# Optimization experiments

Measured on AMD Instinct MI355X. Metric: run time of the kernel, lower is better.

The kernel has to match this reference:

```python
import jax, jax.numpy as jnp
import numpy as np


def _hat(w):
    wx, wy, wz = w[..., 0], w[..., 1], w[..., 2]
    O = jnp.zeros_like(wx)
    return jnp.stack([
        jnp.stack([O, -wz, wy], -1),
        jnp.stack([wz, O, -wx], -1),
        jnp.stack([-wy, wx, O], -1)], -2)


def so3_exp_map(w):
    # w: [B,3] axis-angle -> [B,3,3] rotation (Rodrigues with Taylor fallback)
    th2 = jnp.sum(w * w, -1)[..., None, None]
    th = jnp.sqrt(th2 + 1e-30)
    a = jnp.where(th2 > 1e-8, jnp.sin(th) / th, 1.0 - th2 / 6.0)
    b = jnp.where(th2 > 1e-8, (1.0 - jnp.cos(th)) / th2, 0.5 - th2 / 24.0)
    K = _hat(w)
    I = jnp.eye(3, dtype=w.dtype)
    return I + a * K + b * (K @ K)


def _trilinear(vol, pts):
    # vol: [X,Y,Z]; pts: [N,3] voxel coords; zero outside the volume
    dims = jnp.asarray(vol.shape, dtype=pts.dtype)
    inside = jnp.all((pts >= 0.0) & (pts <= dims - 1.0), axis=-1)
    p0 = jnp.floor(pts)
    f = pts - p0
    hi = jnp.asarray(vol.shape, dtype=jnp.int32) - 1
    i0 = jnp.clip(p0.astype(jnp.int32), 0, hi)
    i1 = jnp.clip(i0 + 1, 0, hi)
    x0, y0, z0 = i0[:, 0], i0[:, 1], i0[:, 2]
    x1, y1, z1 = i1[:, 0], i1[:, 1], i1[:, 2]
    fx, fy, fz = f[:, 0], f[:, 1], f[:, 2]
    gx, gy, gz = 1.0 - fx, 1.0 - fy, 1.0 - fz
    val = (vol[x0, y0, z0] * gx * gy * gz + vol[x1, y0, z0] * fx * gy * gz
           + vol[x0, y1, z0] * gx * fy * gz + vol[x0, y0, z1] * gx * gy * fz
           + vol[x1, y1, z0] * fx * fy * gz + vol[x1, y0, z1] * fx * gy * fz
           + vol[x0, y1, z1] * gx * fy * fz + vol[x1, y1, z1] * fx * fy * fz)
    return jnp.where(inside, val, 0.0)


def setup_inputs() -> dict:
    key = jax.random.key(0)
    k1, k2, k3 = jax.random.split(key, 3)
    D = 256
    volume = jax.random.uniform(k1, (D, D, D), dtype=jnp.float32)
    spacing = jnp.ones(3, dtype=jnp.float32)                    # 1 mm voxels
    origin = jnp.full((3,), -(D - 1) / 2.0, dtype=jnp.float32)  # volume centered at 0
    isocenter = jnp.zeros(3, dtype=jnp.float32)
    sdd = jnp.array([1020.0], dtype=jnp.float32)
    # cam-to-world: source 510 mm behind isocenter on -z axis
    rt_inv = jnp.eye(4, dtype=jnp.float32).at[2, 3].set(-510.0)[None]
    # intrinsics: 512x512 detector, 2 mm pixels -> focal = sdd/pixel = 510
    f = 510.0
    K = jnp.array([[f, 0.0, 256.0], [0.0, f, 256.0], [0.0, 0.0, 1.0]], jnp.float32)
    k_inv = jnp.linalg.inv(K)
    eps = 1e-8
    rot = eps * jax.random.normal(k2, (1, 3), dtype=jnp.float32)
    xyz = eps * jax.random.normal(k3, (1, 3), dtype=jnp.float32)
    return {"volume": volume, "rt_inv": rt_inv, "k_inv": k_inv, "sdd": sdd,
            "isocenter": isocenter, "origin": origin, "spacing": spacing,
            "rot": rot, "xyz": xyz, "height": 512, "width": 512, "n_steps": 256}


def reference(volume, rt_inv, k_inv, sdd, isocenter, origin, spacing, rot, xyz,
              height, width, n_steps):
    dtype = volume.dtype
    # --- pose property: pivot @ exp(rot),R@xyz @ pivot_inv, then rt_inv @ pose ---
    R = so3_exp_map(rot)[0]                       # [3,3]
    t = R @ xyz[0]                                # einsum('bij,bj->bi')
    T = jnp.eye(4, dtype=dtype).at[:3, :3].set(R).at[:3, 3].set(t)
    rtm = rt_inv[0]
    c = (jnp.linalg.inv(rtm) @ jnp.append(isocenter, jnp.ones(1, dtype)))[:3]
    piv = jnp.eye(4, dtype=dtype).at[:3, 3].set(c)
    piv_inv = jnp.eye(4, dtype=dtype).at[:3, 3].set(-c)
    pose = rtm @ (piv @ (T @ piv_inv))            # cam-to-world, [4,4]
    # --- render: ray-march DRR ---
    u = jnp.arange(width, dtype=dtype) + 0.5
    v = jnp.arange(height, dtype=dtype) + 0.5
    uu, vv = jnp.meshgrid(u, v, indexing='xy')    # [H,W]
    pix = jnp.stack([uu.ravel(), vv.ravel(), jnp.ones(height * width, dtype)], -1)
    dir_cam = (pix @ k_inv.T) * sdd[0]            # detector points at depth sdd, cam frame
    Rw, src = pose[:3, :3], pose[:3, 3]
    dirs = dir_cam @ Rw.T                         # world-frame source->detector rays [N,3]
    seglen = jnp.linalg.norm(dirs, axis=-1) / n_steps

    def step(acc, i):
        frac = (i.astype(dtype) + 0.5) / n_steps
        pts = src + dirs * frac                   # [N,3] world points
        vox = (pts - origin) / spacing            # voxel coords
        return acc + _trilinear(volume, vox), None

    acc, _ = jax.lax.scan(step, jnp.zeros(height * width, dtype), jnp.arange(n_steps))
    img = acc * seglen                            # line-integral approximation
    return img.reshape(1, 1, height, width)
```

## Files before the change

kernel.cpp:

```cpp
#include <hip/hip_runtime.h>
#include <hip/hip_fp16.h>

#define W 512
#define H 512
#define NSTEPS 256
#define D 256
#define DM1 255.0f
#define PAIR_WS_BYTES (256ull*256ull*256ull*4ull)

struct SetupOut {
    float Rw[9];
    float src[3];
    float kinv[9];
    float sdd;
    float org[3];
    float invsp[3];
};

__device__ __forceinline__ void mat4mul(const float* A, const float* B, float* C) {
    #pragma unroll
    for (int i = 0; i < 4; ++i)
        #pragma unroll
        for (int j = 0; j < 4; ++j) {
            float s = 0.f;
            #pragma unroll
            for (int k = 0; k < 4; ++k) s += A[i*4+k] * B[k*4+j];
            C[i*4+j] = s;
        }
}

__device__ void compute_setup(const float* rt_inv, const float* k_inv, const float* sdd,
                              const float* isocenter, const float* origin, const float* spacing,
                              const float* rot, const float* xyz, SetupOut* o) {
    float wx = rot[0], wy = rot[1], wz = rot[2];
    float th2 = wx*wx + wy*wy + wz*wz;
    float th = sqrtf(th2 + 1e-30f);
    float a, b;
    if (th2 > 1e-8f) { a = sinf(th) / th; b = (1.f - cosf(th)) / th2; }
    else             { a = 1.f - th2 / 6.f; b = 0.5f - th2 / 24.f; }
    float K[9]  = {0.f,-wz,wy,  wz,0.f,-wx,  -wy,wx,0.f};
    float K2[9];
    #pragma unroll
    for (int i = 0; i < 3; ++i)
        #pragma unroll
        for (int j = 0; j < 3; ++j) {
            float s = 0.f;
            #pragma unroll
            for (int k = 0; k < 3; ++k) s += K[i*3+k] * K[k*3+j];
            K2[i*3+j] = s;
        }
    float R[9];
    #pragma unroll
    for (int i = 0; i < 9; ++i) R[i] = ((i % 4 == 0) ? 1.f : 0.f) + a*K[i] + b*K2[i];
    float t[3];
    #pragma unroll
    for (int i = 0; i < 3; ++i)
        t[i] = R[i*3+0]*xyz[0] + R[i*3+1]*xyz[1] + R[i*3+2]*xyz[2];

    float Ainv[16];
    const float* M = rt_inv;
    if (M[12] == 0.f && M[13] == 0.f && M[14] == 0.f && M[15] == 1.f) {
        const float r00=M[0],r01=M[1],r02=M[2],  r10=M[4],r11=M[5],r12=M[6],
                    r20=M[8],r21=M[9],r22=M[10];
        const float c00 = r11*r22 - r12*r21, c01 = r02*r21 - r01*r22, c02 = r01*r12 - r02*r11;
        const float c10 = r12*r20 - r10*r22, c11 = r00*r22 - r02*r20, c12 = r02*r10 - r00*r12;
        const float c20 = r10*r21 - r11*r20, c21 = r01*r20 - r00*r21, c22 = r00*r11 - r01*r10;
        const float det = r00*c00 + r01*c10 + r02*c20;
        const float id  = 1.f / det;
        const float tx = M[3], ty = M[7], tz = M[11];
        Ainv[0]=c00*id; Ainv[1]=c01*id; Ainv[2]=c02*id;
        Ainv[4]=c10*id; Ainv[5]=c11*id; Ainv[6]=c12*id;
        Ainv[8]=c20*id; Ainv[9]=c21*id; Ainv[10]=c22*id;
        Ainv[3]  = -(Ainv[0]*tx + Ainv[1]*ty + Ainv[2]*tz);
        Ainv[7]  = -(Ainv[4]*tx + Ainv[5]*ty + Ainv[6]*tz);
        Ainv[11] = -(Ainv[8]*tx + Ainv[9]*ty + Ainv[10]*tz);
        Ainv[12]=0.f; Ainv[13]=0.f; Ainv[14]=0.f; Ainv[15]=1.f;
    } else {
        float A[16];
        #pragma unroll
        for (int i = 0; i < 16; ++i) { A[i] = rt_inv[i]; Ainv[i] = 0.f; }
        Ainv[0] = Ainv[5] = Ainv[10] = Ainv[15] = 1.f;
        for (int c = 0; c < 4; ++c) {
            int p = c; float mx = fabsf(A[c*4+c]);
            for (int r = c+1; r < 4; ++r) { float v = fabsf(A[r*4+c]); if (v > mx) { mx = v; p = r; } }
            if (p != c) {
                for (int j = 0; j < 4; ++j) {
                    float tmp = A[c*4+j];   A[c*4+j]   = A[p*4+j];   A[p*4+j]   = tmp;
                    tmp = Ainv[c*4+j];      Ainv[c*4+j] = Ainv[p*4+j]; Ainv[p*4+j] = tmp;
                }
            }
            float inv = 1.f / A[c*4+c];
            for (int j = 0; j < 4; ++j) { A[c*4+j] *= inv; Ainv[c*4+j] *= inv; }
            for (int r = 0; r < 4; ++r) if (r != c) {
                float f = A[r*4+c];
                for (int j = 0; j < 4; ++j) { A[r*4+j] -= f*A[c*4+j]; Ainv[r*4+j] -= f*Ainv[c*4+j]; }
            }
        }
    }
    float cv[3];
    #pragma unroll
    for (int i = 0; i < 3; ++i)
        cv[i] = Ainv[i*4+0]*isocenter[0] + Ainv[i*4+1]*isocenter[1]
              + Ainv[i*4+2]*isocenter[2] + Ainv[i*4+3];

    float T[16]    = {R[0],R[1],R[2],t[0],  R[3],R[4],R[5],t[1],  R[6],R[7],R[8],t[2],  0,0,0,1};
    float piv[16]  = {1,0,0, cv[0],  0,1,0, cv[1],  0,0,1, cv[2],  0,0,0,1};
    float pivi[16] = {1,0,0,-cv[0],  0,1,0,-cv[1],  0,0,1,-cv[2],  0,0,0,1};
    float M1[16], M2[16], pose[16];
    mat4mul(T, pivi, M1);
    mat4mul(piv, M1, M2);
    mat4mul(rt_inv, M2, pose);

    #pragma unroll
    for (int i = 0; i < 3; ++i) {
        #pragma unroll
        for (int j = 0; j < 3; ++j) o->Rw[i*3+j] = pose[i*4+j];
        o->src[i] = pose[i*4+3];
    }
    #pragma unroll
    for (int i = 0; i < 9; ++i) o->kinv[i] = k_inv[i];
    o->sdd = sdd[0];
    #pragma unroll
    for (int i = 0; i < 3; ++i) { o->org[i] = origin[i]; o->invsp[i] = 1.f / spacing[i]; }
}

__global__ __launch_bounds__(256) void setup_kernel2(
    const float* __restrict__ rt_inv, const float* __restrict__ k_inv,
    const float* __restrict__ sdd, const float* __restrict__ isocenter,
    const float* __restrict__ origin, const float* __restrict__ spacing,
    const float* __restrict__ rot, const float* __restrict__ xyz,
    SetupOut* __restrict__ sp, unsigned char* __restrict__ gmask)
{
    __shared__ SetupOut S;
    if (threadIdx.x == 0) {
        compute_setup(rt_inv, k_inv, sdd, isocenter, origin, spacing, rot, xyz, &S);
        *sp = S;
    }
    __syncthreads();
    if (!gmask) return;

    __shared__ unsigned char m[256];
    m[threadIdx.x] = 0;
    __syncthreads();
    {
        const int i = threadIdx.x;
        const float frac = ((float)i + 0.5f) * (1.0f / (float)NSTEPS);
        const float Az = (S.src[2] - S.org[2]) * S.invsp[2];
        float vmin = 1e30f, vmax = -1e30f;
        #pragma unroll
        for (int c = 0; c < 4; ++c) {
            const float u = (c & 1)  ? ((float)W - 0.5f) : 0.5f;
            const float v = (c >> 1) ? ((float)H - 0.5f) : 0.5f;
            const float dcx = (S.kinv[0]*u + S.kinv[1]*v + S.kinv[2]) * S.sdd;
            const float dcy = (S.kinv[3]*u + S.kinv[4]*v + S.kinv[5]) * S.sdd;
            const float dcz = (S.kinv[6]*u + S.kinv[7]*v + S.kinv[8]) * S.sdd;
            const float dz  = S.Rw[6]*dcx + S.Rw[7]*dcy + S.Rw[8]*dcz;
            const float Bz  = dz * S.invsp[2];
            const float vz  = fmaf(Bz, frac, Az);
            vmin = fminf(vmin, vz);
            vmax = fmaxf(vmax, vz);
        }
        const int zlo = max(0,     (int)floorf(vmin - 0.05f));
        const int zhi = min(D - 1, (int)floorf(vmax + 0.05f) + 1);
        for (int z = zlo; z <= zhi; ++z) m[z] = 1;
    }
    __syncthreads();
    gmask[threadIdx.x] = m[threadIdx.x];
}

__global__ __launch_bounds__(256) void repack_pair_t(const float* __restrict__ vol,
                                                     unsigned int* __restrict__ ws,
                                                     const unsigned char* __restrict__ gmask) {
    const int x  = blockIdx.x;
    const int y0 = blockIdx.y * 128;
    const int z0 = blockIdx.z * 64;
    const int tid  = threadIdx.x;

    __shared__ unsigned int tf2[129 * 32];
    __shared__ unsigned char zm[64];
    const int xbase = x << 16;

    if (tid < 64) zm[tid] = gmask ? gmask[z0 + tid] : (unsigned char)1;

    {
        const int s  = tid & 31;
        const int r0 = tid >> 5;
        const bool need = (gmask == nullptr) ||
                          (gmask[z0 + 2*s] | gmask[z0 + 2*s + 1]) != 0;
        if (need) {
            for (int r = r0; r <= 128; r += 8) {
                const int y = min(y0 + r, D - 1);
                const float2 f = reinterpret_cast<const float2*>(vol + xbase + (y << 8) + z0)[s];
                __half2 h = __floats2half2_rn(f.x, f.y);
                tf2[r * 32 + (s ^ (r & 31))] = *reinterpret_cast<unsigned int*>(&h);
            }
        }
    }
    __syncthreads();

    const int grp  = tid >> 6;
    const int lane = tid & 63;
    const int ra = 2 * lane, rb = 2 * lane + 1, rc = 2 * lane + 2;
    for (int w = grp; w < 64; w += 4) {
        if (!zm[w]) continue;
        const int wp = w >> 1;
        const int sh = (w & 1) << 4;
        const unsigned int ha = (tf2[ra * 32 + (wp ^ (ra & 31))] >> sh) & 0xffffu;
        const unsigned int hb = (tf2[rb * 32 + (wp ^ (rb & 31))] >> sh) & 0xffffu;
        const unsigned int hc = (tf2[rc * 32 + (wp ^ (rc & 31))] >> sh) & 0xffffu;
        uint2 q;
        q.x = ha | (hb << 16);
        q.y = hb | (hc << 16);
        *reinterpret_cast<uint2*>(ws + xbase + ((z0 + w) << 8) + y0 + ra) = q;
    }
}

struct RayState {
    float Ax, Ay, Az, Bx, By, Bz, seglen;
    int imin, imax;
    bool any;
};

__device__ __forceinline__ RayState ray_setup(const SetupOut* S, int ix, int iy) {
    RayState r;
    const float u = (float)ix + 0.5f;
    const float v = (float)iy + 0.5f;
    const float dcx = (S->kinv[0]*u + S->kinv[1]*v + S->kinv[2]) * S->sdd;
    const float dcy = (S->kinv[3]*u + S->kinv[4]*v + S->kinv[5]) * S->sdd;
    const float dcz = (S->kinv[6]*u + S->kinv[7]*v + S->kinv[8]) * S->sdd;
    const float dx = S->Rw[0]*dcx + S->Rw[1]*dcy + S->Rw[2]*dcz;
    const float dy = S->Rw[3]*dcx + S->Rw[4]*dcy + S->Rw[5]*dcz;
    const float dz = S->Rw[6]*dcx + S->Rw[7]*dcy + S->Rw[8]*dcz;
    r.seglen = sqrtf(dx*dx + dy*dy + dz*dz) * (1.0f / (float)NSTEPS);
    r.Ax = (S->src[0] - S->org[0]) * S->invsp[0];
    r.Ay = (S->src[1] - S->org[1]) * S->invsp[1];
    r.Az = (S->src[2] - S->org[2]) * S->invsp[2];
    r.Bx = dx * S->invsp[0];
    r.By = dy * S->invsp[1];
    r.Bz = dz * S->invsp[2];

    float fmin = 0.f, fmax = 1.f;
    bool empty = false;
    const float aa[3] = { r.Ax, r.Ay, r.Az };
    const float bb[3] = { r.Bx, r.By, r.Bz };
    #pragma unroll
    for (int k = 0; k < 3; ++k) {
        if (fabsf(bb[k]) > 1e-12f) {
            const float rcp = 1.f / bb[k];
            const float t0 = (0.f - aa[k]) * rcp;
            const float t1 = (DM1 - aa[k]) * rcp;
            fmin = fmaxf(fmin, fminf(t0, t1));
            fmax = fminf(fmax, fmaxf(t0, t1));
        } else if (aa[k] < 0.f || aa[k] > DM1) {
            empty = true;
        }
    }
    r.any = !empty && (fmax >= fmin);
    r.imin = max(0,          (int)floorf(fmin * (float)NSTEPS - 0.5f) - 1);
    r.imax = min(NSTEPS - 1, (int)ceilf (fmax * (float)NSTEPS - 0.5f) + 1);
    return r;
}

__global__ __launch_bounds__(256) void drr_pair_kernel(
    const unsigned int* __restrict__ wsp, const SetupOut* __restrict__ S,
    float* __restrict__ out)
{
    const int b   = blockIdx.x;
    const int xcd = b & 7;
    const int j   = b >> 3;
    const int uu  = xcd * 16 + (j & 15);
    const int vv  = j >> 4;

    const int seg = threadIdx.x & 3;
    const int iy = vv * 16 + (threadIdx.x >> 2);
    const int ix = uu * 4  + threadIdx.y;
    const RayState r = ray_setup(S, ix, iy);

    float acc = 0.f;
    if (r.any) {
        #pragma unroll 4
        for (int i = r.imin + seg; i <= r.imax; i += 4) {
            const float frac = ((float)i + 0.5f) * (1.0f / (float)NSTEPS);
            const float vx = fmaf(r.Bx, frac, r.Ax);
            const float vy = fmaf(r.By, frac, r.Ay);
            const float vz = fmaf(r.Bz, frac, r.Az);
            const bool inside = (vx >= 0.f) && (vx <= DM1) &&
                                (vy >= 0.f) && (vy <= DM1) &&
                                (vz >= 0.f) && (vz <= DM1);
            const float cx = fminf(fmaxf(vx, 0.f), DM1);
            const float cy = fminf(fmaxf(vy, 0.f), DM1);
            const float cz = fminf(fmaxf(vz, 0.f), DM1);
            const float px = floorf(cx), py = floorf(cy), pz = floorf(cz);
            const int x0 = (int)px, y0 = (int)py, z0 = (int)pz;
            const int x1 = min(x0 + 1, D - 1);
            const int z1 = min(z0 + 1, D - 1);
            const float fx = cx - px, fy = cy - py, fz = cz - pz;
            const float gx = 1.f - fx, gy = 1.f - fy, gz = 1.f - fz;

            const int e00 = (x0 << 16) + (z0 << 8) + y0;
            const int zo  = (z1 - z0) << 8;
            const int xo  = (x1 - x0) << 16;

            const unsigned int q00 = wsp[e00];
            const unsigned int q01 = wsp[e00 + zo];
            const unsigned int q10 = wsp[e00 + xo];
            const unsigned int q11 = wsp[e00 + xo + zo];

            const float2 a00 = __half22float2(*reinterpret_cast<const __half2*>(&q00));
            const float2 a01 = __half22float2(*reinterpret_cast<const __half2*>(&q01));
            const float2 a10 = __half22float2(*reinterpret_cast<const __half2*>(&q10));
            const float2 a11 = __half22float2(*reinterpret_cast<const __half2*>(&q11));

            const float m00 = a00.x*gy + a00.y*fy;
            const float m01 = a01.x*gy + a01.y*fy;
            const float m10 = a10.x*gy + a10.y*fy;
            const float m11 = a11.x*gy + a11.y*fy;
            const float c0 = m00*gz + m01*fz;
            const float c1 = m10*gz + m11*fz;
            const float samp = c0*gx + c1*fx;
            acc += inside ? samp : 0.f;
        }
    }
    acc += __shfl_xor(acc, 1);
    acc += __shfl_xor(acc, 2);
    if (seg == 0)
        out[iy * W + ix] = acc * r.seglen;
}

__global__ __launch_bounds__(256) void drr_direct_kernel(
    const float* __restrict__ vol,
    const float* __restrict__ rt_inv, const float* __restrict__ k_inv,
    const float* __restrict__ sdd, const float* __restrict__ isocenter,
    const float* __restrict__ origin, const float* __restrict__ spacing,
    const float* __restrict__ rot, const float* __restrict__ xyz,
    float* __restrict__ out)
{
    __shared__ SetupOut S;
    if (threadIdx.x == 0 && threadIdx.y == 0)
        compute_setup(rt_inv, k_inv, sdd, isocenter, origin, spacing, rot, xyz, &S);
    __syncthreads();

    const int seg = threadIdx.x & 1;
    const int iy = blockIdx.x * 32 + (threadIdx.x >> 1);
    const int ix = blockIdx.y * 4  + threadIdx.y;
    const RayState r = ray_setup(&S, ix, iy);

    float acc = 0.f;
    if (r.any) {
        #pragma unroll 4
        for (int i = r.imin + seg; i <= r.imax; i += 2) {
            const float frac = ((float)i + 0.5f) * (1.0f / (float)NSTEPS);
            const float vx = fmaf(r.Bx, frac, r.Ax);
            const float vy = fmaf(r.By, frac, r.Ay);
            const float vz = fmaf(r.Bz, frac, r.Az);
            const bool inside = (vx >= 0.f) && (vx <= DM1) &&
                                (vy >= 0.f) && (vy <= DM1) &&
                                (vz >= 0.f) && (vz <= DM1);
            const float cx = fminf(fmaxf(vx, 0.f), DM1);
            const float cy = fminf(fmaxf(vy, 0.f), DM1);
            const float cz = fminf(fmaxf(vz, 0.f), DM1);
            const float px = floorf(cx), py = floorf(cy), pz = floorf(cz);
            const int x0 = (int)px, y0 = (int)py, z0 = (int)pz;
            const int x1 = min(x0 + 1, D - 1);
            const int y1 = min(y0 + 1, D - 1);
            const int z1 = min(z0 + 1, D - 1);
            const float fx = cx - px, fy = cy - py, fz = cz - pz;
            const float gx = 1.f - fx, gy = 1.f - fy, gz = 1.f - fz;

            const int base = (x0 << 16) + (y0 << 8);
            const int bx = (x1 - x0) << 16;
            const int by = (y1 - y0) << 8;

            const float v000 = vol[base + z0],           v001 = vol[base + z1];
            const float v010 = vol[base + by + z0],      v011 = vol[base + by + z1];
            const float v100 = vol[base + bx + z0],      v101 = vol[base + bx + z1];
            const float v110 = vol[base + bx + by + z0], v111 = vol[base + bx + by + z1];

            const float c00 = v000*gz + v001*fz;
            const float c01 = v010*gz + v011*fz;
            const float c10 = v100*gz + v101*fz;
            const float c11 = v110*gz + v111*fz;
            const float samp = (c00*gy + c01*fy)*gx + (c10*gy + c11*fy)*fx;
            acc += inside ? samp : 0.f;
        }
    }
    acc += __shfl_xor(acc, 1);
    if (seg == 0)
        out[iy * W + ix] = acc * r.seglen;
}

extern "C" void kernel_launch(void* const* d_in, const int* in_sizes, int n_in,
                              void* d_out, int out_size, void* d_ws, size_t ws_size,
                              hipStream_t stream) {
    const float* vol      = (const float*)d_in[0];
    const float* rt_inv   = (const float*)d_in[1];
    const float* k_inv    = (const float*)d_in[2];
    const float* sdd      = (const float*)d_in[3];
    const float* iso      = (const float*)d_in[4];
    const float* origin   = (const float*)d_in[5];
    const float* spacing  = (const float*)d_in[6];
    const float* rot      = (const float*)d_in[7];
    const float* xyz      = (const float*)d_in[8];
    float* out = (float*)d_out;

    if (ws_size >= PAIR_WS_BYTES + 4096) {
        unsigned int* wsp = (unsigned int*)d_ws;
        SetupOut* sp = (SetupOut*)((char*)d_ws + PAIR_WS_BYTES);
        unsigned char* gmask = (unsigned char*)d_ws + PAIR_WS_BYTES + 512;

        setup_kernel2<<<1, 256, 0, stream>>>(rt_inv, k_inv, sdd, iso, origin,
                                             spacing, rot, xyz, sp, gmask);
        repack_pair_t<<<dim3(D, 2, 4), 256, 0, stream>>>(vol, wsp, gmask);
        drr_pair_kernel<<<dim3(4096), dim3(64, 4), 0, stream>>>(wsp, sp, out);
    } else {
        drr_direct_kernel<<<dim3(H / 32, W / 4), dim3(64, 4), 0, stream>>>(
            vol, rt_inv, k_inv, sdd, iso, origin, spacing, rot, xyz, out);
    }
}
```

Baseline: 53.77 us.

## Fold setup kernel into repack and render kernels, compact z-slice list

Removes the single-block setup kernel launch by having each repack and render block recompute the pose/setup on one thread into shared memory. Each repack block now computes its own z-band mask and builds a compacted list of needed z slices, so the write loop iterates only active slices. This drops one kernel launch and its serialization, at the cost of redundant per-block setup math and extra barriers in both kernels.

```diff
diff --git a/kernel.cpp b/kernel.cpp
--- a/kernel.cpp
+++ b/kernel.cpp
@@ -124,69 +124,71 @@
     for (int i = 0; i < 3; ++i) { o->org[i] = origin[i]; o->invsp[i] = 1.f / spacing[i]; }
 }
 
-__global__ __launch_bounds__(256) void setup_kernel2(
+__device__ __forceinline__ void step_zband(const SetupOut& S, int i, int* zlo, int* zhi) {
+    const float frac = ((float)i + 0.5f) * (1.0f / (float)NSTEPS);
+    const float Az = (S.src[2] - S.org[2]) * S.invsp[2];
+    float vmin = 1e30f, vmax = -1e30f;
+    #pragma unroll
+    for (int c = 0; c < 4; ++c) {
+        const float u = (c & 1)  ? ((float)W - 0.5f) : 0.5f;
+        const float v = (c >> 1) ? ((float)H - 0.5f) : 0.5f;
+        const float dcx = (S.kinv[0]*u + S.kinv[1]*v + S.kinv[2]) * S.sdd;
+        const float dcy = (S.kinv[3]*u + S.kinv[4]*v + S.kinv[5]) * S.sdd;
+        const float dcz = (S.kinv[6]*u + S.kinv[7]*v + S.kinv[8]) * S.sdd;
+        const float dz  = S.Rw[6]*dcx + S.Rw[7]*dcy + S.Rw[8]*dcz;
+        const float Bz  = dz * S.invsp[2];
+        const float vz  = fmaf(Bz, frac, Az);
+        vmin = fminf(vmin, vz);
+        vmax = fmaxf(vmax, vz);
+    }
+    *zlo = max(0,     (int)floorf(vmin - 0.05f));
+    *zhi = min(D - 1, (int)floorf(vmax + 0.05f) + 1);
+}
+
+__global__ __launch_bounds__(256) void repack_pair_t(
+    const float* __restrict__ vol, unsigned int* __restrict__ ws,
     const float* __restrict__ rt_inv, const float* __restrict__ k_inv,
     const float* __restrict__ sdd, const float* __restrict__ isocenter,
     const float* __restrict__ origin, const float* __restrict__ spacing,
-    const float* __restrict__ rot, const float* __restrict__ xyz,
-    SetupOut* __restrict__ sp, unsigned char* __restrict__ gmask)
+    const float* __restrict__ rot, const float* __restrict__ xyz)
 {
-    __shared__ SetupOut S;
-    if (threadIdx.x == 0) {
-        compute_setup(rt_inv, k_inv, sdd, isocenter, origin, spacing, rot, xyz, &S);
-        *sp = S;
-    }
-    __syncthreads();
-    if (!gmask) return;
-
-    __shared__ unsigned char m[256];
-    m[threadIdx.x] = 0;
-    __syncthreads();
-    {
-        const int i = threadIdx.x;
-        const float frac = ((float)i + 0.5f) * (1.0f / (float)NSTEPS);
-        const float Az = (S.src[2] - S.org[2]) * S.invsp[2];
-        float vmin = 1e30f, vmax = -1e30f;
-        #pragma unroll
-        for (int c = 0; c < 4; ++c) {
-            const float u = (c & 1)  ? ((float)W - 0.5f) : 0.5f;
-            const float v = (c >> 1) ? ((float)H - 0.5f) : 0.5f;
-            const float dcx = (S.kinv[0]*u + S.kinv[1]*v + S.kinv[2]) * S.sdd;
-            const float dcy = (S.kinv[3]*u + S.kinv[4]*v + S.kinv[5]) * S.sdd;
-            const float dcz = (S.kinv[6]*u + S.kinv[7]*v + S.kinv[8]) * S.sdd;
-            const float dz  = S.Rw[6]*dcx + S.Rw[7]*dcy + S.Rw[8]*dcz;
-            const float Bz  = dz * S.invsp[2];
-            const float vz  = fmaf(Bz, frac, Az);
-            vmin = fminf(vmin, vz);
-            vmax = fmaxf(vmax, vz);
-        }
-        const int zlo = max(0,     (int)floorf(vmin - 0.05f));
-        const int zhi = min(D - 1, (int)floorf(vmax + 0.05f) + 1);
-        for (int z = zlo; z <= zhi; ++z) m[z] = 1;
-    }
-    __syncthreads();
-    gmask[threadIdx.x] = m[threadIdx.x];
-}
-
-__global__ __launch_bounds__(256) void repack_pair_t(const float* __restrict__ vol,
-                                                     unsigned int* __restrict__ ws,
-                                                     const unsigned char* __restrict__ gmask) {
     const int x  = blockIdx.x;
     const int y0 = blockIdx.y * 128;
     const int z0 = blockIdx.z * 64;
     const int tid  = threadIdx.x;
 
+    __shared__ SetupOut S;
     __shared__ unsigned int tf2[129 * 32];
     __shared__ unsigned char zm[64];
+    __shared__ unsigned char zlist[64];
+    __shared__ int nz;
+
+    if (tid == 0)
+        compute_setup(rt_inv, k_inv, sdd, isocenter, origin, spacing, rot, xyz, &S);
+    if (tid < 64) zm[tid] = 0;
+    __syncthreads();
+
+    {
+        int zlo, zhi;
+        step_zband(S, tid, &zlo, &zhi);
+        zlo = max(zlo, z0);
+        zhi = min(zhi, z0 + 63);
+        for (int z = zlo; z <= zhi; ++z) zm[z - z0] = 1;
+    }
+    __syncthreads();
+    if (tid == 0) {
+        int n = 0;
+        for (int w = 0; w < 64; ++w) if (zm[w]) zlist[n++] = (unsigned char)w;
+        nz = n;
+    }
+    __syncthreads();
+
     const int xbase = x << 16;
-
-    if (tid < 64) zm[tid] = gmask ? gmask[z0 + tid] : (unsigned char)1;
 
     {
         const int s  = tid & 31;
         const int r0 = tid >> 5;
-        const bool need = (gmask == nullptr) ||
-                          (gmask[z0 + 2*s] | gmask[z0 + 2*s + 1]) != 0;
+        const bool need = (zm[2*s] | zm[2*s + 1]) != 0;
         if (need) {
             for (int r = r0; r <= 128; r += 8) {
                 const int y = min(y0 + r, D - 1);
@@ -201,8 +203,9 @@
     const int grp  = tid >> 6;
     const int lane = tid & 63;
     const int ra = 2 * lane, rb = 2 * lane + 1, rc = 2 * lane + 2;
-    for (int w = grp; w < 64; w += 4) {
-        if (!zm[w]) continue;
+    const int count = nz;
+    for (int k = grp; k < count; k += 4) {
+        const int w  = zlist[k];
         const int wp = w >> 1;
         const int sh = (w & 1) << 4;
         const unsigned int ha = (tf2[ra * 32 + (wp ^ (ra & 31))] >> sh) & 0xffffu;
@@ -262,9 +265,18 @@
 }
 
 __global__ __launch_bounds__(256) void drr_pair_kernel(
-    const unsigned int* __restrict__ wsp, const SetupOut* __restrict__ S,
+    const unsigned int* __restrict__ wsp,
+    const float* __restrict__ rt_inv, const float* __restrict__ k_inv,
+    const float* __restrict__ sdd, const float* __restrict__ isocenter,
+    const float* __restrict__ origin, const float* __restrict__ spacing,
+    const float* __restrict__ rot, const float* __restrict__ xyz,
     float* __restrict__ out)
 {
+    __shared__ SetupOut S;
+    if (threadIdx.x == 0 && threadIdx.y == 0)
+        compute_setup(rt_inv, k_inv, sdd, isocenter, origin, spacing, rot, xyz, &S);
+    __syncthreads();
+
     const int b   = blockIdx.x;
     const int xcd = b & 7;
     const int j   = b >> 3;
@@ -274,7 +286,7 @@
     const int seg = threadIdx.x & 3;
     const int iy = vv * 16 + (threadIdx.x >> 2);
     const int ix = uu * 4  + threadIdx.y;
-    const RayState r = ray_setup(S, ix, iy);
+    const RayState r = ray_setup(&S, ix, iy);
 
     float acc = 0.f;
     if (r.any) {
@@ -403,15 +415,12 @@
     const float* xyz      = (const float*)d_in[8];
     float* out = (float*)d_out;
 
-    if (ws_size >= PAIR_WS_BYTES + 4096) {
+    if (ws_size >= PAIR_WS_BYTES) {
         unsigned int* wsp = (unsigned int*)d_ws;
-        SetupOut* sp = (SetupOut*)((char*)d_ws + PAIR_WS_BYTES);
-        unsigned char* gmask = (unsigned char*)d_ws + PAIR_WS_BYTES + 512;
-
-        setup_kernel2<<<1, 256, 0, stream>>>(rt_inv, k_inv, sdd, iso, origin,
-                                             spacing, rot, xyz, sp, gmask);
-        repack_pair_t<<<dim3(D, 2, 4), 256, 0, stream>>>(vol, wsp, gmask);
-        drr_pair_kernel<<<dim3(4096), dim3(64, 4), 0, stream>>>(wsp, sp, out);
+        repack_pair_t<<<dim3(D, 2, 4), 256, 0, stream>>>(
+            vol, wsp, rt_inv, k_inv, sdd, iso, origin, spacing, rot, xyz);
+        drr_pair_kernel<<<dim3(4096), dim3(64, 4), 0, stream>>>(
+            wsp, rt_inv, k_inv, sdd, iso, origin, spacing, rot, xyz, out);
     } else {
         drr_direct_kernel<<<dim3(H / 32, W / 4), dim3(64, 4), 0, stream>>>(
             vol, rt_inv, k_inv, sdd, iso, origin, spacing, rot, xyz, out);
```

Result: slower. 82.69 us (+53.8%).
